# Kernel tuning notes

Measured on AMD Instinct MI355X. Metric: run time of the kernel, lower is better.

Reference implementation:

```python
import jax, jax.numpy as jnp
import numpy as np

IN_DIM = 128
OUT_DIM = 128
ATTN_DIM = 64
N_REL = 200
N_NODE = 50000
N_EDGE = 500000
N_QUERY = 64
COE_TIMEDIFF = 0.2  # computed in torch code but unused downstream


def setup_inputs() -> dict:
    key = jax.random.key(0)
    ks = jax.random.split(key, 24)
    # edges: [E,7] with columns (r_idx, _, rel, _, tau, sub, obj)
    r_idx = jax.random.randint(ks[0], (N_EDGE,), 0, N_QUERY)
    rel = jax.random.randint(ks[1], (N_EDGE,), 0, 2 * N_REL + 1)
    tau = jax.random.randint(ks[2], (N_EDGE,), -1, 366)  # -1 triggers the where() fallback
    sub = jax.random.randint(ks[3], (N_EDGE,), 0, N_NODE)
    obj = jax.random.randint(ks[4], (N_EDGE,), 0, N_NODE)
    fill = jnp.zeros((N_EDGE,), jnp.int64 if jax.config.jax_enable_x64 else jnp.int32)
    edges = jnp.stack([r_idx, fill, rel, fill, tau, sub, obj], axis=1)
    s = 1.0 / np.sqrt(IN_DIM)
    sa = 1.0 / np.sqrt(ATTN_DIM)
    return {
        "q_sub": jax.random.randint(ks[5], (N_QUERY,), 0, N_NODE),
        "q_rel": jax.random.randint(ks[6], (N_QUERY,), 0, 2 * N_REL + 1),
        "q_tau": jax.random.randint(ks[7], (N_QUERY,), 0, 366),
        "hidden": jax.random.normal(ks[8], (N_NODE, IN_DIM), jnp.float32),
        "edges": edges,
        "n_node": N_NODE,
        "old_nodes_new_idx": jax.random.randint(ks[9], (10000,), 0, N_NODE),
        "rela_embed": jax.random.normal(ks[10], (2 * N_REL + 1, IN_DIM), jnp.float32),
        "Ws": jax.random.normal(ks[11], (IN_DIM, ATTN_DIM), jnp.float32) * s,
        "Wr": jax.random.normal(ks[12], (IN_DIM, ATTN_DIM), jnp.float32) * s,
        "Wqr_W": jax.random.normal(ks[13], (IN_DIM, ATTN_DIM), jnp.float32) * s,
        "Wqr_b": jax.random.normal(ks[14], (ATTN_DIM,), jnp.float32) * s,
        "Wtau": jax.random.normal(ks[15], (IN_DIM, ATTN_DIM), jnp.float32) * s,
        "w_alpha_W": jax.random.normal(ks[16], (ATTN_DIM, 1), jnp.float32) * sa,
        "w_alpha_b": jax.random.normal(ks[17], (1,), jnp.float32) * sa,
        "Wh": jax.random.normal(ks[18], (IN_DIM, OUT_DIM), jnp.float32) * s,
        "wt1": jax.random.normal(ks[19], (1, IN_DIM), jnp.float32),
        "bt1": jax.random.normal(ks[20], (1, IN_DIM), jnp.float32),
        "wt2": jax.random.normal(ks[21], (1, IN_DIM), jnp.float32),
        "bt2": jax.random.normal(ks[22], (1, IN_DIM), jnp.float32),
    }


def reference(q_sub, q_rel, q_tau, hidden, edges, n_node, old_nodes_new_idx,
              rela_embed, Ws, Wr, Wqr_W, Wqr_b, Wtau, w_alpha_W, w_alpha_b,
              Wh, wt1, bt1, wt2, bt2):
    r_idx = edges[:, 0]
    rel = edges[:, 2]
    tau = edges[:, 4]
    sub = edges[:, 5]
    obj = edges[:, 6]
    hs = hidden[sub]                      # [E, in_dim] gather
    hr = rela_embed[rel]                  # [E, in_dim]
    h_qr = rela_embed[q_rel][r_idx]       # [E, in_dim]
    taus_q = q_tau[r_idx]
    tau = jnp.where(tau >= 0, tau, taus_q)
    delta_tau = (tau - taus_q).astype(hidden.dtype)[:, None]  # [E,1]
    h_tau = wt1 * delta_tau + bt1 + jnp.sin(wt2 * delta_tau + bt2)  # [E, in_dim]
    message = hs + hr + h_tau
    pre = jax.nn.relu(hs @ Ws + hr @ Wr + (h_qr @ Wqr_W + Wqr_b) + h_tau @ Wtau)
    alpha = jax.nn.sigmoid(pre @ w_alpha_W + w_alpha_b)  # [E,1]
    msg_agg = jax.ops.segment_sum(alpha * message, obj, num_segments=n_node)
    return msg_agg @ Wh  # act is identity by default
```

## Files before the change

### kernel.cpp

```cpp
#include <hip/hip_runtime.h>
#include <hip/hip_fp16.h>

#define IN_DIM   128
#define OUT_DIM  128
#define ATTN_DIM 64
#define N_RELV   401
#define N_NODE   50000
#define N_EDGE   500000
#define N_QUERY  64
#define N_DT     731
#define CAP      40

#define NB_NODE  782
#define NB_RELDT 566
#define NB_QR    32
#define NB_TOT   (NB_NODE + NB_RELDT + NB_QR + 1)

typedef unsigned short ushort_t;
typedef unsigned int   uint_t;
typedef __attribute__((ext_vector_type(8))) short v8s;
typedef __attribute__((ext_vector_type(4))) float v4f;

__device__ __forceinline__ int clampi(int v, int lo, int hi) {
    return v < lo ? lo : (v > hi ? hi : v);
}
__device__ __forceinline__ float bu2f(ushort_t u) {
    union { uint_t i; float f; } v; v.i = ((uint_t)u) << 16; return v.f;
}
__device__ __forceinline__ float blo(uint_t u) { return bu2f((ushort_t)(u & 0xffff)); }
__device__ __forceinline__ float bhi(uint_t u) { return bu2f((ushort_t)(u >> 16)); }
__device__ __forceinline__ ushort_t f2bu(float f) {
    union { float f; uint_t i; } v; v.f = f;
    const uint_t x = v.i;
    return (ushort_t)((x + 0x7fffu + ((x >> 16) & 1u)) >> 16);
}
__device__ __forceinline__ uint_t cvtpk(float a, float b) {
    uint_t r;
    asm("v_cvt_pk_bf16_f32 %0, %1, %2" : "=v"(r) : "v"(a), "v"(b));
    return r;
}

__device__ __forceinline__ void parse_edge(const int* __restrict__ edges, int e,
                                           int i64, int& r, int& rel, int& tau,
                                           int& sub, int& obj) {
    if (i64) {
        const int* E = edges + (size_t)e * 14;
        r = E[0]; rel = E[4]; tau = E[8]; sub = E[10]; obj = E[12];
    } else {
        const int* E = edges + (size_t)e * 7;
        r = E[0]; rel = E[2]; tau = E[4]; sub = E[5]; obj = E[6];
    }
    r   = clampi(r,   0, N_QUERY - 1);
    rel = clampi(rel, 0, N_RELV - 1);
    sub = clampi(sub, 0, N_NODE - 1);
    obj = clampi(obj, 0, N_NODE - 1);
}

__device__ __forceinline__ int swz_byte(int row, int byte_in_row) {
    return (row * 256 + byte_in_row) ^ ((row & 7) << 4);
}

__global__ __launch_bounds__(256) void fused_pre(
    const float* __restrict__ hidden, const float* __restrict__ Ws,
    const float* __restrict__ Wh,   const float* __restrict__ rela,
    const float* __restrict__ Wr,   const float* __restrict__ Wtau,
    const float* __restrict__ wt1,  const float* __restrict__ bt1,
    const float* __restrict__ wt2,  const float* __restrict__ bt2,
    const int* __restrict__ q_rel,  const float* __restrict__ WqrW,
    const float* __restrict__ Wqrb, const int* __restrict__ edges,
    ushort_t* __restrict__ node_attn, ushort_t* __restrict__ node_msg,
    ushort_t* __restrict__ rel_attn,  ushort_t* __restrict__ rel_msg,
    ushort_t* __restrict__ dt_attn,   ushort_t* __restrict__ dt_msg,
    ushort_t* __restrict__ Xqr,
    int* __restrict__ flag, int* __restrict__ cnt, int* __restrict__ ovfn)
{
    __shared__ ushort_t shw[192 * 128];
    const int bid = blockIdx.x, tid = threadIdx.x;

    if (bid < NB_NODE) {
        #pragma unroll
        for (int i = 0; i < 4; ++i) {
            const int pi = tid + 256 * i;
            const int kp = pi >> 4;
            const int n4 = (pi & 15) * 4;
            const float4 A = *(const float4*)(Ws + (size_t)(2 * kp) * 64 + n4);
            const float4 B = *(const float4*)(Ws + (size_t)(2 * kp + 1) * 64 + n4);
            const float Aa[4] = {A.x, A.y, A.z, A.w};
            const float Bа[4] = {B.x, B.y, B.z, B.w};
            #pragma unroll
            for (int j = 0; j < 4; ++j) {
                const int row = n4 + j;
                const uint_t u = (uint_t)f2bu(Aa[j]) | ((uint_t)f2bu(Bа[j]) << 16);
                *(uint_t*)((char*)shw + swz_byte(row, kp * 4)) = u;
            }
        }
        #pragma unroll
        for (int i = 0; i < 8; ++i) {
            const int pi = tid + 256 * i;
            const int kp = pi >> 5;
            const int n4 = (pi & 31) * 4;
            const float4 A = *(const float4*)(Wh + (size_t)(2 * kp) * 128 + n4);
            const float4 B = *(const float4*)(Wh + (size_t)(2 * kp + 1) * 128 + n4);
            const float Aa[4] = {A.x, A.y, A.z, A.w};
            const float Bа[4] = {B.x, B.y, B.z, B.w};
            #pragma unroll
            for (int j = 0; j < 4; ++j) {
                const int row = 64 + n4 + j;
                const uint_t u = (uint_t)f2bu(Aa[j]) | ((uint_t)f2bu(Bа[j]) << 16);
                *(uint_t*)((char*)shw + swz_byte(row, kp * 4)) = u;
            }
        }
        __syncthreads();

        const int wid  = tid >> 6;
        const int lane = tid & 63;
        const int m16  = lane & 15;
        const int q    = lane >> 4;
        const int nb   = bid * 64;
        const int row  = nb + wid * 16 + m16;
        const int rowc = row < N_NODE ? row : N_NODE - 1;

        v8s hfr[4];
        #pragma unroll
        for (int c = 0; c < 4; ++c) {
            const float4 f0 = *(const float4*)(hidden + (size_t)rowc * 128 + 32 * c + 8 * q);
            const float4 f1 = *(const float4*)(hidden + (size_t)rowc * 128 + 32 * c + 8 * q + 4);
            union { v8s s; uint4 u; } uu;
            uu.u = make_uint4(cvtpk(f0.x, f0.y), cvtpk(f0.z, f0.w),
                              cvtpk(f1.x, f1.y), cvtpk(f1.z, f1.w));
            hfr[c] = uu.s;
        }

        #pragma unroll
        for (int t = 0; t < 12; ++t) {
            v4f acc = {0.f, 0.f, 0.f, 0.f};
            #pragma unroll
            for (int c = 0; c < 4; ++c) {
                const v8s wfr = *(const v8s*)((const char*)shw +
                                  swz_byte(16 * t + m16, (32 * c + 8 * q) * 2));
                acc = __builtin_amdgcn_mfma_f32_16x16x32_bf16(wfr, hfr[c], acc, 0, 0, 0);
            }
            if (row < N_NODE) {
                const uint_t u0 = cvtpk(acc[0], acc[1]);
                const uint_t u1 = cvtpk(acc[2], acc[3]);
                const int dim = 16 * t + 4 * q;
                if (dim < 64) {
                    *(uint2*)(node_attn + (size_t)row * 64 + dim) = make_uint2(u0, u1);
                } else {
                    *(uint2*)(node_msg + (size_t)row * 128 + (dim - 64)) = make_uint2(u0, u1);
                }
            }
        }
    } else if (bid < NB_NODE + NB_RELDT) {
        const int bid2   = bid - NB_NODE;
        const int half   = tid >> 7;
        const int t128   = tid & 127;
        const int rowid  = bid2 * 2 + half;
        float* h = (float*)shw + half * 128;

        if (rowid < N_RELV) {
            h[t128] = rela[(size_t)rowid * IN_DIM + t128];
        } else {
            const float dtv = (float)((rowid - N_RELV) - 365);
            h[t128] = wt1[t128] * dtv + bt1[t128] + sinf(wt2[t128] * dtv + bt2[t128]);
        }
        __syncthreads();

        if (rowid < N_RELV) {
            if (t128 < ATTN_DIM) {
                float a = 0.f;
                #pragma unroll 8
                for (int d = 0; d < IN_DIM; ++d) a += h[d] * Wr[d * ATTN_DIM + t128];
                rel_attn[(size_t)rowid * ATTN_DIM + t128] = f2bu(a);
            }
            float m = 0.f;
            #pragma unroll 8
            for (int d = 0; d < IN_DIM; ++d) m += h[d] * Wh[d * OUT_DIM + t128];
            rel_msg[(size_t)rowid * OUT_DIM + t128] = f2bu(m);
        } else {
            const int i = rowid - N_RELV;
            if (t128 < ATTN_DIM) {
                float a = 0.f;
                #pragma unroll 8
                for (int d = 0; d < IN_DIM; ++d) a += h[d] * Wtau[d * ATTN_DIM + t128];
                dt_attn[(size_t)i * ATTN_DIM + t128] = f2bu(a);
            }
            float m = 0.f;
            #pragma unroll 8
            for (int d = 0; d < IN_DIM; ++d) m += h[d] * Wh[d * OUT_DIM + t128];
            dt_msg[(size_t)i * OUT_DIM + t128] = f2bu(m);
        }
        const int z = bid2 * 89 + tid;
        if (tid < 89 && z < N_NODE) cnt[z] = 0;
    } else if (bid < NB_NODE + NB_RELDT + NB_QR) {
        const int bid3 = bid - NB_NODE - NB_RELDT;
        const int half = tid >> 7;
        const int t128 = tid & 127;
        float* h  = (float*)shw + half * 128;
        int*   ok = (int*)((float*)shw + 512);

        if (tid == 0) *ok = 1;
        __syncthreads();
        const int w = edges[2 * tid + 1];
        if (w != 0 && w != -1) *ok = 0;
        __syncthreads();
        const int i64 = *ok;

        const int qn  = bid3 * 2 + half;
        const int rel = clampi(q_rel[i64 ? 2 * qn : qn], 0, N_RELV - 1);
        h[t128] = rela[(size_t)rel * IN_DIM + t128];
        __syncthreads();
        if (t128 < ATTN_DIM) {
            float acc = Wqrb[t128];
            #pragma unroll 8
            for (int d = 0; d < IN_DIM; ++d) acc += h[d] * WqrW[d * ATTN_DIM + t128];
            Xqr[(size_t)qn * ATTN_DIM + t128] = f2bu(acc);
        }
    } else {
        int* ok = (int*)shw;
        if (tid == 0) *ok = 0;
        __syncthreads();
        int badv = 0;
        for (int t = tid; t < 1000; t += 256) {
            const int w = edges[2 * t + 1];
            if (w != 0 && w != -1) badv = 1;
        }
        if (badv) *ok = 1;
        __syncthreads();
        if (tid == 0) { flag[0] = (*ok == 0) ? 1 : 0; ovfn[0] = 0; }
    }
}

__device__ __forceinline__ float dot8(uint4 xs, uint4 xr, uint4 xt, uint4 xq,
                                      float4 wA, float4 wB)
{
    float s0, s1, v;
    s0 = blo(xs.x) + blo(xr.x) + blo(xt.x) + blo(xq.x);
    s1 = bhi(xs.x) + bhi(xr.x) + bhi(xt.x) + bhi(xq.x);
    v  = fmaxf(s0, 0.f) * wA.x + fmaxf(s1, 0.f) * wA.y;
    s0 = blo(xs.y) + blo(xr.y) + blo(xt.y) + blo(xq.y);
    s1 = bhi(xs.y) + bhi(xr.y) + bhi(xt.y) + bhi(xq.y);
    v += fmaxf(s0, 0.f) * wA.z + fmaxf(s1, 0.f) * wA.w;
    s0 = blo(xs.z) + blo(xr.z) + blo(xt.z) + blo(xq.z);
    s1 = bhi(xs.z) + bhi(xr.z) + bhi(xt.z) + bhi(xq.z);
    v += fmaxf(s0, 0.f) * wB.x + fmaxf(s1, 0.f) * wB.y;
    s0 = blo(xs.w) + blo(xr.w) + blo(xt.w) + blo(xq.w);
    s1 = bhi(xs.w) + bhi(xr.w) + bhi(xt.w) + bhi(xq.w);
    v += fmaxf(s0, 0.f) * wB.z + fmaxf(s1, 0.f) * wB.w;
    return v;
}

__global__ __launch_bounds__(256) void alpha_scatter(
    const int* __restrict__ edges, const int* __restrict__ q_tau,
    const ushort_t* __restrict__ node_attn, const ushort_t* __restrict__ rel_attn,
    const ushort_t* __restrict__ dt_attn,  const ushort_t* __restrict__ Xqr,
    const float* __restrict__ w_alpha_W, const float* __restrict__ w_alpha_b,
    const int* __restrict__ flag, int* __restrict__ cnt,
    int2* __restrict__ meta, int* __restrict__ ovfn, int4* __restrict__ ovfl)
{
    const int g   = threadIdx.x & 7;
    const int grp = threadIdx.x >> 3;
    const int e0  = blockIdx.x * 128 + grp * 4;
    const int i64 = flag[0];

    const float4 wA = *(const float4*)(w_alpha_W + 8 * g);
    const float4 wB = *(const float4*)(w_alpha_W + 8 * g + 4);

    const int ec0 = e0     < N_EDGE ? e0     : N_EDGE - 1;
    const int ec1 = e0 + 1 < N_EDGE ? e0 + 1 : N_EDGE - 1;
    const int ec2 = e0 + 2 < N_EDGE ? e0 + 2 : N_EDGE - 1;
    const int ec3 = e0 + 3 < N_EDGE ? e0 + 3 : N_EDGE - 1;

    int r0, rel0, tau0, sub0, obj0; parse_edge(edges, ec0, i64, r0, rel0, tau0, sub0, obj0);
    int r1, rel1, tau1, sub1, obj1; parse_edge(edges, ec1, i64, r1, rel1, tau1, sub1, obj1);
    int r2, rel2, tau2, sub2, obj2; parse_edge(edges, ec2, i64, r2, rel2, tau2, sub2, obj2);
    int r3, rel3, tau3, sub3, obj3; parse_edge(edges, ec3, i64, r3, rel3, tau3, sub3, obj3);
    const int tq0 = q_tau[i64 ? 2 * r0 : r0];
    const int tq1 = q_tau[i64 ? 2 * r1 : r1];
    const int tq2 = q_tau[i64 ? 2 * r2 : r2];
    const int tq3 = q_tau[i64 ? 2 * r3 : r3];
    if (tau0 < 0) tau0 = tq0;
    if (tau1 < 0) tau1 = tq1;
    if (tau2 < 0) tau2 = tq2;
    if (tau3 < 0) tau3 = tq3;
    const int di0 = clampi(tau0 - tq0 + 365, 0, N_DT - 1);
    const int di1 = clampi(tau1 - tq1 + 365, 0, N_DT - 1);
    const int di2 = clampi(tau2 - tq2 + 365, 0, N_DT - 1);
    const int di3 = clampi(tau3 - tq3 + 365, 0, N_DT - 1);

    const uint4 xs0 = *(const uint4*)(node_attn + (size_t)sub0 * ATTN_DIM + 8 * g);
    const uint4 xr0 = *(const uint4*)(rel_attn + (size_t)rel0 * ATTN_DIM + 8 * g);
    const uint4 xt0 = *(const uint4*)(dt_attn  + (size_t)di0  * ATTN_DIM + 8 * g);
    const uint4 xq0 = *(const uint4*)(Xqr      + (size_t)r0   * ATTN_DIM + 8 * g);
    const uint4 xs1 = *(const uint4*)(node_attn + (size_t)sub1 * ATTN_DIM + 8 * g);
    const uint4 xr1 = *(const uint4*)(rel_attn + (size_t)rel1 * ATTN_DIM + 8 * g);
    const uint4 xt1 = *(const uint4*)(dt_attn  + (size_t)di1  * ATTN_DIM + 8 * g);
    const uint4 xq1 = *(const uint4*)(Xqr      + (size_t)r1   * ATTN_DIM + 8 * g);
    const uint4 xs2 = *(const uint4*)(node_attn + (size_t)sub2 * ATTN_DIM + 8 * g);
    const uint4 xr2 = *(const uint4*)(rel_attn + (size_t)rel2 * ATTN_DIM + 8 * g);
    const uint4 xt2 = *(const uint4*)(dt_attn  + (size_t)di2  * ATTN_DIM + 8 * g);
    const uint4 xq2 = *(const uint4*)(Xqr      + (size_t)r2   * ATTN_DIM + 8 * g);
    const uint4 xs3 = *(const uint4*)(node_attn + (size_t)sub3 * ATTN_DIM + 8 * g);
    const uint4 xr3 = *(const uint4*)(rel_attn + (size_t)rel3 * ATTN_DIM + 8 * g);
    const uint4 xt3 = *(const uint4*)(dt_attn  + (size_t)di3  * ATTN_DIM + 8 * g);
    const uint4 xq3 = *(const uint4*)(Xqr      + (size_t)r3   * ATTN_DIM + 8 * g);

    float v0 = dot8(xs0, xr0, xt0, xq0, wA, wB);
    float v1 = dot8(xs1, xr1, xt1, xq1, wA, wB);
    float v2 = dot8(xs2, xr2, xt2, xq2, wA, wB);
    float v3 = dot8(xs3, xr3, xt3, xq3, wA, wB);

    #pragma unroll
    for (int off = 4; off > 0; off >>= 1) {
        v0 += __shfl_xor(v0, off, 8);
        v1 += __shfl_xor(v1, off, 8);
        v2 += __shfl_xor(v2, off, 8);
        v3 += __shfl_xor(v3, off, 8);
    }

    if (g < 4 && e0 + g < N_EDGE) {
        const float vg  = g == 0 ? v0 : (g == 1 ? v1 : (g == 2 ? v2 : v3));
        const int objg  = g == 0 ? obj0 : (g == 1 ? obj1 : (g == 2 ? obj2 : obj3));
        const int subg  = g == 0 ? sub0 : (g == 1 ? sub1 : (g == 2 ? sub2 : sub3));
        const int dig   = g == 0 ? di0  : (g == 1 ? di1  : (g == 2 ? di2  : di3));
        const int relg  = g == 0 ? rel0 : (g == 1 ? rel1 : (g == 2 ? rel2 : rel3));
        const float alpha = 1.f / (1.f + __expf(-(vg + w_alpha_b[0])));
        const int pos = atomicAdd(&cnt[objg], 1);
        if (pos < CAP) {
            const uint_t px = (uint_t)subg | ((uint_t)dig << 17) | ((uint_t)(relg & 31) << 27);
            const uint_t py = (uint_t)(relg >> 5) |
                              ((uint_t)__half_as_ushort(__float2half_rn(alpha)) << 16);
            meta[(size_t)pos * N_NODE + objg] = make_int2((int)px, (int)py);
        } else {
            const int ov = atomicAdd(ovfn, 1);
            if (ov < N_EDGE)
                ovfl[ov] = make_int4(subg | (dig << 17), relg | (objg << 9),
                                     __float_as_int(alpha), 0);
        }
    }
}

__device__ __forceinline__ void agg_edge(
    int2 m, int l32,
    const ushort_t* __restrict__ node_msg, const ushort_t* __restrict__ rel_msg,
    const ushort_t* __restrict__ dt_msg,
    float& a0, float& a1, float& a2, float& a3)
{
    const int sub = m.x & 0x1FFFF;
    const int di  = ((uint_t)m.x >> 17) & 0x3FF;
    const int rel = (((uint_t)m.x >> 27) & 31) | (((uint_t)m.y & 0xF) << 5);
    const float al = __half2float(__ushort_as_half((ushort_t)((uint_t)m.y >> 16)));
    const uint2 am = *(const uint2*)(node_msg + (size_t)sub * 128 + 4 * l32);
    const uint2 bm = *(const uint2*)(rel_msg  + (size_t)rel * 128 + 4 * l32);
    const uint2 tm = *(const uint2*)(dt_msg   + (size_t)di  * 128 + 4 * l32);
    a0 += al * (blo(am.x) + blo(bm.x) + blo(tm.x));
    a1 += al * (bhi(am.x) + bhi(bm.x) + bhi(tm.x));
    a2 += al * (blo(am.y) + blo(bm.y) + blo(tm.y));
    a3 += al * (bhi(am.y) + bhi(bm.y) + bhi(tm.y));
}

__global__ __launch_bounds__(256) void agg_kernel(
    const int* __restrict__ cnt, const int2* __restrict__ meta,
    const int* __restrict__ ovfn, const int4* __restrict__ ovfl,
    const ushort_t* __restrict__ node_msg, const ushort_t* __restrict__ rel_msg,
    const ushort_t* __restrict__ dt_msg, float* __restrict__ out)
{
    const int lane = threadIdx.x & 63;
    const int half = lane >> 5;
    const int l32  = lane & 31;
    const int n    = blockIdx.x * 4 + (threadIdx.x >> 6);

    int m = cnt[n]; if (m > CAP) m = CAP;
    float a0 = 0.f, a1 = 0.f, a2 = 0.f, a3 = 0.f;

    int j = 0;
    for (; j + 3 < m; j += 4) {
        const int2 ma = meta[(size_t)(j + half) * N_NODE + n];
        const int2 mb = meta[(size_t)(j + 2 + half) * N_NODE + n];
        agg_edge(ma, l32, node_msg, rel_msg, dt_msg, a0, a1, a2, a3);
        agg_edge(mb, l32, node_msg, rel_msg, dt_msg, a0, a1, a2, a3);
    }
    for (; j + 1 < m; j += 2) {
        const int2 ma = meta[(size_t)(j + half) * N_NODE + n];
        agg_edge(ma, l32, node_msg, rel_msg, dt_msg, a0, a1, a2, a3);
    }
    if (j < m && half == 0) {
        const int2 ma = meta[(size_t)j * N_NODE + n];
        agg_edge(ma, l32, node_msg, rel_msg, dt_msg, a0, a1, a2, a3);
    }

    int nov = ovfn[0]; if (nov > N_EDGE) nov = N_EDGE;
    for (int i = 0; i < nov; ++i) {
        const int4 mo = ovfl[i];
        const int objo = (int)((uint_t)mo.y >> 9);
        if (objo != n || half != 0) continue;
        const int subo = mo.x & 0x1FFFF;
        const int dio  = (int)((uint_t)mo.x >> 17);
        const int relo = mo.y & 0x1FF;
        const float alo = __int_as_float(mo.z);
        const uint2 am = *(const uint2*)(node_msg + (size_t)subo * 128 + 4 * l32);
        const uint2 bm = *(const uint2*)(rel_msg  + (size_t)relo * 128 + 4 * l32);
        const uint2 tm = *(const uint2*)(dt_msg   + (size_t)dio  * 128 + 4 * l32);
        a0 += alo * (blo(am.x) + blo(bm.x) + blo(tm.x));
        a1 += alo * (bhi(am.x) + bhi(bm.x) + bhi(tm.x));
        a2 += alo * (blo(am.y) + blo(bm.y) + blo(tm.y));
        a3 += alo * (bhi(am.y) + bhi(bm.y) + bhi(tm.y));
    }

    a0 += __shfl_xor(a0, 32, 64);
    a1 += __shfl_xor(a1, 32, 64);
    a2 += __shfl_xor(a2, 32, 64);
    a3 += __shfl_xor(a3, 32, 64);

    if (half == 0) {
        float4 o; o.x = a0; o.y = a1; o.z = a2; o.w = a3;
        *(float4*)(out + (size_t)n * OUT_DIM + 4 * l32) = o;
    }
}

__global__ __launch_bounds__(256) void edge_atomic_kernel(
    const int* __restrict__ edges, const int* __restrict__ q_tau,
    const ushort_t* __restrict__ node_attn, const ushort_t* __restrict__ node_msg,
    const ushort_t* __restrict__ rel_attn,  const ushort_t* __restrict__ rel_msg,
    const ushort_t* __restrict__ dt_attn,   const ushort_t* __restrict__ dt_msg,
    const ushort_t* __restrict__ Xqr,
    const float* __restrict__ w_alpha_W, const float* __restrict__ w_alpha_b,
    const int* __restrict__ flag, float* __restrict__ out)
{
    const int lane = threadIdx.x & 63;
    const int e    = blockIdx.x * 4 + (threadIdx.x >> 6);
    const int i64  = flag[0];

    int r, rel, tau, sub, obj;
    parse_edge(edges, e, i64, r, rel, tau, sub, obj);
    const int tq = q_tau[i64 ? 2 * r : r];
    if (tau < 0) tau = tq;
    const int di = clampi(tau - tq + 365, 0, N_DT - 1);

    const float xs = bu2f(node_attn[(size_t)sub * ATTN_DIM + lane]);
    const float xr = bu2f(rel_attn[(size_t)rel * ATTN_DIM + lane]);
    const float xt = bu2f(dt_attn[(size_t)di  * ATTN_DIM + lane]);
    const float xq = bu2f(Xqr[(size_t)r * ATTN_DIM + lane]);

    float v = fmaxf(xs + xr + xq + xt, 0.f) * w_alpha_W[lane];
    #pragma unroll
    for (int off = 32; off > 0; off >>= 1)
        v += __shfl_down(v, off, 64);
    v = __shfl(v, 0, 64);
    const float alpha = 1.f / (1.f + __expf(-(v + w_alpha_b[0])));

    const uint_t am = *(const uint_t*)(node_msg + (size_t)sub * 128 + 2 * lane);
    const uint_t bm = *(const uint_t*)(rel_msg  + (size_t)rel * 128 + 2 * lane);
    const uint_t tm = *(const uint_t*)(dt_msg   + (size_t)di  * 128 + 2 * lane);
    const float mx = blo(am) + blo(bm) + blo(tm);
    const float my = bhi(am) + bhi(bm) + bhi(tm);

    float* dst = out + (size_t)obj * OUT_DIM;
    atomicAdd(dst + 2 * lane,     alpha * mx);
    atomicAdd(dst + 2 * lane + 1, alpha * my);
}

extern "C" void kernel_launch(void* const* d_in, const int* in_sizes, int n_in,
                              void* d_out, int out_size, void* d_ws, size_t ws_size,
                              hipStream_t stream)
{
    const int*   q_rel  = (const int*)d_in[1];
    const int*   q_tau  = (const int*)d_in[2];
    const float* hidden = (const float*)d_in[3];
    const int*   edges  = (const int*)d_in[4];
    const float* rela   = (const float*)d_in[7];
    const float* Ws     = (const float*)d_in[8];
    const float* Wr     = (const float*)d_in[9];
    const float* WqrW   = (const float*)d_in[10];
    const float* Wqrb   = (const float*)d_in[11];
    const float* Wtau   = (const float*)d_in[12];
    const float* waW    = (const float*)d_in[13];
    const float* wab    = (const float*)d_in[14];
    const float* Wh     = (const float*)d_in[15];
    const float* wt1    = (const float*)d_in[16];
    const float* bt1    = (const float*)d_in[17];
    const float* wt2    = (const float*)d_in[18];
    const float* bt2    = (const float*)d_in[19];
    float* out = (float*)d_out;

    char* p = (char*)d_ws;
    size_t off = 0;
    auto carve = [&](size_t bytes) {
        char* q = p + off;
        off = (off + bytes + 255) & ~(size_t)255;
        return q;
    };
    int*      flag      = (int*)     carve(64);
    int*      cnt       = (int*)     carve((size_t)N_NODE * 4);
    int*      ovfn      = (int*)     carve(64);
    ushort_t* XqrB      = (ushort_t*)carve((size_t)N_QUERY * ATTN_DIM * 2);
    ushort_t* rel_attn  = (ushort_t*)carve((size_t)N_RELV * ATTN_DIM * 2);
    ushort_t* rel_msg   = (ushort_t*)carve((size_t)N_RELV * OUT_DIM * 2);
    ushort_t* dt_attn   = (ushort_t*)carve((size_t)N_DT * ATTN_DIM * 2);
    ushort_t* dt_msg    = (ushort_t*)carve((size_t)N_DT * OUT_DIM * 2);
    ushort_t* node_attn = (ushort_t*)carve((size_t)N_NODE * ATTN_DIM * 2);
    ushort_t* node_msg  = (ushort_t*)carve((size_t)N_NODE * OUT_DIM * 2);
    int2*     meta      = (int2*)    carve((size_t)N_NODE * CAP * 8);
    int4*     ovfl      = (int4*)    carve((size_t)N_EDGE * 16);
    const size_t need_full = off;

    fused_pre<<<NB_TOT, 256, 0, stream>>>(
        hidden, Ws, Wh, rela, Wr, Wtau, wt1, bt1, wt2, bt2,
        q_rel, WqrW, Wqrb, edges,
        node_attn, node_msg, rel_attn, rel_msg, dt_attn, dt_msg, XqrB,
        flag, cnt, ovfn);

    if (ws_size >= need_full) {
        alpha_scatter<<<(N_EDGE + 127) / 128, 256, 0, stream>>>(
            edges, q_tau, node_attn, rel_attn, dt_attn, XqrB,
            waW, wab, flag, cnt, meta, ovfn, ovfl);
        agg_kernel<<<N_NODE / 4, 256, 0, stream>>>(cnt, meta, ovfn, ovfl,
                                                   node_msg, rel_msg, dt_msg, out);
    } else {
        (void)hipMemsetAsync(out, 0, (size_t)out_size * sizeof(float), stream);
        edge_atomic_kernel<<<N_EDGE / 4, 256, 0, stream>>>(edges, q_tau,
                                                           node_attn, node_msg,
                                                           rel_attn, rel_msg,
                                                           dt_attn, dt_msg, XqrB,
                                                           waW, wab, flag, out);
    }
}
```

Measured before the change: 200.2 us.

## Move relation, time-delta and query projections onto MFMA and vectorize edge loads

The scalar per-row dot-product blocks for relation, time-delta and query projections are replaced with MFMA bf16 tiles that reuse the node-projection path. Fewer blocks handle these tables and the count buffer is zeroed with int4 stores. The edge kernel reads each group's 4 edges with one int4 load per lane plus shuffles instead of scalar strided loads. The aggregation loop is unrolled to 8 edges. Projections of the small tables now run in bf16 rather than fp32, which slightly changes precision, and the i64 format check now samples more edges.

```diff
diff --git a/kernel.cpp b/kernel.cpp
--- a/kernel.cpp
+++ b/kernel.cpp
@@ -11,10 +11,17 @@
 #define N_DT     731
 #define CAP      40
 
-#define NB_NODE  782
-#define NB_RELDT 566
-#define NB_QR    32
-#define NB_TOT   (NB_NODE + NB_RELDT + NB_QR + 1)
+#define NBW_NODE 782
+#define NBW_REL  7
+#define NBW_DT   12
+#define NBW_QR   1
+#define NBW_ZERO 13
+#define RB0      NBW_NODE
+#define DB0      (NBW_NODE + NBW_REL)
+#define QB0      (DB0 + NBW_DT)
+#define ZB0      (QB0 + NBW_QR)
+#define FB0      (ZB0 + NBW_ZERO)
+#define NB_TOT   (FB0 + 1)
 
 typedef unsigned short ushort_t;
 typedef unsigned int   uint_t;
@@ -40,24 +47,78 @@
     return r;
 }
 
-__device__ __forceinline__ void parse_edge(const int* __restrict__ edges, int e,
-                                           int i64, int& r, int& rel, int& tau,
-                                           int& sub, int& obj) {
-    if (i64) {
-        const int* E = edges + (size_t)e * 14;
-        r = E[0]; rel = E[4]; tau = E[8]; sub = E[10]; obj = E[12];
-    } else {
-        const int* E = edges + (size_t)e * 7;
-        r = E[0]; rel = E[2]; tau = E[4]; sub = E[5]; obj = E[6];
-    }
-    r   = clampi(r,   0, N_QUERY - 1);
-    rel = clampi(rel, 0, N_RELV - 1);
-    sub = clampi(sub, 0, N_NODE - 1);
-    obj = clampi(obj, 0, N_NODE - 1);
-}
-
 __device__ __forceinline__ int swz_byte(int row, int byte_in_row) {
     return (row * 256 + byte_in_row) ^ ((row & 7) << 4);
+}
+
+__device__ __forceinline__ void stage_w64(ushort_t* shw, const float* __restrict__ W,
+                                          int tid) {
+    #pragma unroll
+    for (int i = 0; i < 4; ++i) {
+        const int pi = tid + 256 * i;
+        const int kp = pi >> 4;
+        const int n4 = (pi & 15) * 4;
+        const float4 A = *(const float4*)(W + (size_t)(2 * kp) * 64 + n4);
+        const float4 B = *(const float4*)(W + (size_t)(2 * kp + 1) * 64 + n4);
+        const float Aa[4] = {A.x, A.y, A.z, A.w};
+        const float Ba[4] = {B.x, B.y, B.z, B.w};
+        #pragma unroll
+        for (int j = 0; j < 4; ++j)
+            *(uint_t*)((char*)shw + swz_byte(n4 + j, kp * 4)) = cvtpk(Aa[j], Ba[j]);
+    }
+}
+__device__ __forceinline__ void stage_w128(ushort_t* shw, const float* __restrict__ W,
+                                           int tid) {
+    #pragma unroll
+    for (int i = 0; i < 8; ++i) {
+        const int pi = tid + 256 * i;
+        const int kp = pi >> 5;
+        const int n4 = (pi & 31) * 4;
+        const float4 A = *(const float4*)(W + (size_t)(2 * kp) * 128 + n4);
+        const float4 B = *(const float4*)(W + (size_t)(2 * kp + 1) * 128 + n4);
+        const float Aa[4] = {A.x, A.y, A.z, A.w};
+        const float Ba[4] = {B.x, B.y, B.z, B.w};
+        #pragma unroll
+        for (int j = 0; j < 4; ++j)
+            *(uint_t*)((char*)shw + swz_byte(64 + n4 + j, kp * 4)) = cvtpk(Aa[j], Ba[j]);
+    }
+}
+__device__ __forceinline__ void load_x_rows(const float* __restrict__ X, int rowc,
+                                            int q, v8s hfr[4]) {
+    #pragma unroll
+    for (int c = 0; c < 4; ++c) {
+        const float4 f0 = *(const float4*)(X + (size_t)rowc * 128 + 32 * c + 8 * q);
+        const float4 f1 = *(const float4*)(X + (size_t)rowc * 128 + 32 * c + 8 * q + 4);
+        union { v8s s; uint4 u; } uu;
+        uu.u = make_uint4(cvtpk(f0.x, f0.y), cvtpk(f0.z, f0.w),
+                          cvtpk(f1.x, f1.y), cvtpk(f1.z, f1.w));
+        hfr[c] = uu.s;
+    }
+}
+__device__ __forceinline__ void mfma_store(const ushort_t* shw, const v8s hfr[4],
+                                           int row, int Nlim,
+                                           ushort_t* __restrict__ attn_out,
+                                           ushort_t* __restrict__ msg_out,
+                                           int m16, int q) {
+    #pragma unroll
+    for (int t = 0; t < 12; ++t) {
+        v4f acc = {0.f, 0.f, 0.f, 0.f};
+        #pragma unroll
+        for (int c = 0; c < 4; ++c) {
+            const v8s wfr = *(const v8s*)((const char*)shw +
+                              swz_byte(16 * t + m16, (32 * c + 8 * q) * 2));
+            acc = __builtin_amdgcn_mfma_f32_16x16x32_bf16(wfr, hfr[c], acc, 0, 0, 0);
+        }
+        if (row < Nlim) {
+            const uint_t u0 = cvtpk(acc[0], acc[1]);
+            const uint_t u1 = cvtpk(acc[2], acc[3]);
+            const int dim = 16 * t + 4 * q;
+            if (dim < 64)
+                *(uint2*)(attn_out + (size_t)row * 64 + dim) = make_uint2(u0, u1);
+            else
+                *(uint2*)(msg_out + (size_t)row * 128 + (dim - 64)) = make_uint2(u0, u1);
+        }
+    }
 }
 
 __global__ __launch_bounds__(256) void fused_pre(
@@ -76,63 +137,77 @@
 {
     __shared__ ushort_t shw[192 * 128];
     const int bid = blockIdx.x, tid = threadIdx.x;
-
-    if (bid < NB_NODE) {
-        #pragma unroll
-        for (int i = 0; i < 4; ++i) {
-            const int pi = tid + 256 * i;
-            const int kp = pi >> 4;
-            const int n4 = (pi & 15) * 4;
-            const float4 A = *(const float4*)(Ws + (size_t)(2 * kp) * 64 + n4);
-            const float4 B = *(const float4*)(Ws + (size_t)(2 * kp + 1) * 64 + n4);
-            const float Aa[4] = {A.x, A.y, A.z, A.w};
-            const float Bа[4] = {B.x, B.y, B.z, B.w};
-            #pragma unroll
-            for (int j = 0; j < 4; ++j) {
-                const int row = n4 + j;
-                const uint_t u = (uint_t)f2bu(Aa[j]) | ((uint_t)f2bu(Bа[j]) << 16);
-                *(uint_t*)((char*)shw + swz_byte(row, kp * 4)) = u;
-            }
-        }
-        #pragma unroll
-        for (int i = 0; i < 8; ++i) {
-            const int pi = tid + 256 * i;
-            const int kp = pi >> 5;
-            const int n4 = (pi & 31) * 4;
-            const float4 A = *(const float4*)(Wh + (size_t)(2 * kp) * 128 + n4);
-            const float4 B = *(const float4*)(Wh + (size_t)(2 * kp + 1) * 128 + n4);
-            const float Aa[4] = {A.x, A.y, A.z, A.w};
-            const float Bа[4] = {B.x, B.y, B.z, B.w};
-            #pragma unroll
-            for (int j = 0; j < 4; ++j) {
-                const int row = 64 + n4 + j;
-                const uint_t u = (uint_t)f2bu(Aa[j]) | ((uint_t)f2bu(Bа[j]) << 16);
-                *(uint_t*)((char*)shw + swz_byte(row, kp * 4)) = u;
-            }
-        }
-        __syncthreads();
-
-        const int wid  = tid >> 6;
-        const int lane = tid & 63;
-        const int m16  = lane & 15;
-        const int q    = lane >> 4;
-        const int nb   = bid * 64;
-        const int row  = nb + wid * 16 + m16;
+    const int wid = tid >> 6, lane = tid & 63;
+    const int m16 = lane & 15, q = lane >> 4;
+
+    if (bid < NBW_NODE) {
+        stage_w64 (shw, Ws, tid);
+        stage_w128(shw, Wh, tid);
+        __syncthreads();
+        const int row  = bid * 64 + wid * 16 + m16;
         const int rowc = row < N_NODE ? row : N_NODE - 1;
-
+        v8s hfr[4];
+        load_x_rows(hidden, rowc, q, hfr);
+        mfma_store(shw, hfr, row, N_NODE, node_attn, node_msg, m16, q);
+    } else if (bid < DB0) {
+        stage_w64 (shw, Wr, tid);
+        stage_w128(shw, Wh, tid);
+        __syncthreads();
+        const int row  = (bid - RB0) * 64 + wid * 16 + m16;
+        const int rowc = row < N_RELV ? row : N_RELV - 1;
+        v8s hfr[4];
+        load_x_rows(rela, rowc, q, hfr);
+        mfma_store(shw, hfr, row, N_RELV, rel_attn, rel_msg, m16, q);
+    } else if (bid < QB0) {
+        stage_w64 (shw, Wtau, tid);
+        stage_w128(shw, Wh, tid);
+        __syncthreads();
+        const int row  = (bid - DB0) * 64 + wid * 16 + m16;
+        const int rowc = row < N_DT ? row : N_DT - 1;
+        const float dtv = (float)(rowc - 365);
         v8s hfr[4];
         #pragma unroll
         for (int c = 0; c < 4; ++c) {
-            const float4 f0 = *(const float4*)(hidden + (size_t)rowc * 128 + 32 * c + 8 * q);
-            const float4 f1 = *(const float4*)(hidden + (size_t)rowc * 128 + 32 * c + 8 * q + 4);
+            const int o = 32 * c + 8 * q;
+            const float4 w1a = *(const float4*)(wt1 + o), w1b = *(const float4*)(wt1 + o + 4);
+            const float4 b1a = *(const float4*)(bt1 + o), b1b = *(const float4*)(bt1 + o + 4);
+            const float4 w2a = *(const float4*)(wt2 + o), w2b = *(const float4*)(wt2 + o + 4);
+            const float4 b2a = *(const float4*)(bt2 + o), b2b = *(const float4*)(bt2 + o + 4);
+            const float h0 = w1a.x * dtv + b1a.x + sinf(w2a.x * dtv + b2a.x);
+            const float h1 = w1a.y * dtv + b1a.y + sinf(w2a.y * dtv + b2a.y);
+            const float h2 = w1a.z * dtv + b1a.z + sinf(w2a.z * dtv + b2a.z);
+            const float h3 = w1a.w * dtv + b1a.w + sinf(w2a.w * dtv + b2a.w);
+            const float h4 = w1b.x * dtv + b1b.x + sinf(w2b.x * dtv + b2b.x);
+            const float h5 = w1b.y * dtv + b1b.y + sinf(w2b.y * dtv + b2b.y);
+            const float h6 = w1b.z * dtv + b1b.z + sinf(w2b.z * dtv + b2b.z);
+            const float h7 = w1b.w * dtv + b1b.w + sinf(w2b.w * dtv + b2b.w);
             union { v8s s; uint4 u; } uu;
-            uu.u = make_uint4(cvtpk(f0.x, f0.y), cvtpk(f0.z, f0.w),
-                              cvtpk(f1.x, f1.y), cvtpk(f1.z, f1.w));
+            uu.u = make_uint4(cvtpk(h0, h1), cvtpk(h2, h3), cvtpk(h4, h5), cvtpk(h6, h7));
             hfr[c] = uu.s;
         }
-
+        mfma_store(shw, hfr, row, N_DT, dt_attn, dt_msg, m16, q);
+    } else if (bid < ZB0) {
+        int* ok = (int*)shw;
+        if (tid == 0) *ok = 1;
+        __syncthreads();
+        int badv = 0;
+        for (int t = tid; t < 1000; t += 256) {
+            const int w = edges[2 * t + 1];
+            if (w != 0 && w != -1) badv = 1;
+        }
+        if (badv) *ok = 0;
+        __syncthreads();
+        const int i64 = *ok;
+        __syncthreads();
+
+        stage_w64(shw, WqrW, tid);
+        __syncthreads();
+        const int qrow = wid * 16 + m16;
+        const int relq = clampi(q_rel[i64 ? 2 * qrow : qrow], 0, N_RELV - 1);
+        v8s hfr[4];
+        load_x_rows(rela, relq, q, hfr);
         #pragma unroll
-        for (int t = 0; t < 12; ++t) {
+        for (int t = 0; t < 4; ++t) {
             v4f acc = {0.f, 0.f, 0.f, 0.f};
             #pragma unroll
             for (int c = 0; c < 4; ++c) {
@@ -140,81 +215,19 @@
                                   swz_byte(16 * t + m16, (32 * c + 8 * q) * 2));
                 acc = __builtin_amdgcn_mfma_f32_16x16x32_bf16(wfr, hfr[c], acc, 0, 0, 0);
             }
-            if (row < N_NODE) {
-                const uint_t u0 = cvtpk(acc[0], acc[1]);
-                const uint_t u1 = cvtpk(acc[2], acc[3]);
-                const int dim = 16 * t + 4 * q;
-                if (dim < 64) {
-                    *(uint2*)(node_attn + (size_t)row * 64 + dim) = make_uint2(u0, u1);
-                } else {
-                    *(uint2*)(node_msg + (size_t)row * 128 + (dim - 64)) = make_uint2(u0, u1);
-                }
-            }
-        }
-    } else if (bid < NB_NODE + NB_RELDT) {
-        const int bid2   = bid - NB_NODE;
-        const int half   = tid >> 7;
-        const int t128   = tid & 127;
-        const int rowid  = bid2 * 2 + half;
-        float* h = (float*)shw + half * 128;
-
-        if (rowid < N_RELV) {
-            h[t128] = rela[(size_t)rowid * IN_DIM + t128];
-        } else {
-            const float dtv = (float)((rowid - N_RELV) - 365);
-            h[t128] = wt1[t128] * dtv + bt1[t128] + sinf(wt2[t128] * dtv + bt2[t128]);
-        }
-        __syncthreads();
-
-        if (rowid < N_RELV) {
-            if (t128 < ATTN_DIM) {
-                float a = 0.f;
-                #pragma unroll 8
-                for (int d = 0; d < IN_DIM; ++d) a += h[d] * Wr[d * ATTN_DIM + t128];
-                rel_attn[(size_t)rowid * ATTN_DIM + t128] = f2bu(a);
-            }
-            float m = 0.f;
-            #pragma unroll 8
-            for (int d = 0; d < IN_DIM; ++d) m += h[d] * Wh[d * OUT_DIM + t128];
-            rel_msg[(size_t)rowid * OUT_DIM + t128] = f2bu(m);
-        } else {
-            const int i = rowid - N_RELV;
-            if (t128 < ATTN_DIM) {
-                float a = 0.f;
-                #pragma unroll 8
-                for (int d = 0; d < IN_DIM; ++d) a += h[d] * Wtau[d * ATTN_DIM + t128];
-                dt_attn[(size_t)i * ATTN_DIM + t128] = f2bu(a);
-            }
-            float m = 0.f;
-            #pragma unroll 8
-            for (int d = 0; d < IN_DIM; ++d) m += h[d] * Wh[d * OUT_DIM + t128];
-            dt_msg[(size_t)i * OUT_DIM + t128] = f2bu(m);
-        }
-        const int z = bid2 * 89 + tid;
-        if (tid < 89 && z < N_NODE) cnt[z] = 0;
-    } else if (bid < NB_NODE + NB_RELDT + NB_QR) {
-        const int bid3 = bid - NB_NODE - NB_RELDT;
-        const int half = tid >> 7;
-        const int t128 = tid & 127;
-        float* h  = (float*)shw + half * 128;
-        int*   ok = (int*)((float*)shw + 512);
-
-        if (tid == 0) *ok = 1;
-        __syncthreads();
-        const int w = edges[2 * tid + 1];
-        if (w != 0 && w != -1) *ok = 0;
-        __syncthreads();
-        const int i64 = *ok;
-
-        const int qn  = bid3 * 2 + half;
-        const int rel = clampi(q_rel[i64 ? 2 * qn : qn], 0, N_RELV - 1);
-        h[t128] = rela[(size_t)rel * IN_DIM + t128];
-        __syncthreads();
-        if (t128 < ATTN_DIM) {
-            float acc = Wqrb[t128];
-            #pragma unroll 8
-            for (int d = 0; d < IN_DIM; ++d) acc += h[d] * WqrW[d * ATTN_DIM + t128];
-            Xqr[(size_t)qn * ATTN_DIM + t128] = f2bu(acc);
+            const int dim = 16 * t + 4 * q;
+            const float4 bi = *(const float4*)(Wqrb + dim);
+            const uint_t u0 = cvtpk(acc[0] + bi.x, acc[1] + bi.y);
+            const uint_t u1 = cvtpk(acc[2] + bi.z, acc[3] + bi.w);
+            *(uint2*)(Xqr + (size_t)qrow * 64 + dim) = make_uint2(u0, u1);
+        }
+    } else if (bid < FB0) {
+        int4* c4 = (int4*)cnt;
+        const int b = (bid - ZB0) * 256 + tid;
+        #pragma unroll
+        for (int k = 0; k < 4; ++k) {
+            const int i4 = b * 4 + k;
+            if (i4 < N_NODE / 4) c4[i4] = make_int4(0, 0, 0, 0);
         }
     } else {
         int* ok = (int*)shw;
@@ -260,21 +273,43 @@
 {
     const int g   = threadIdx.x & 7;
     const int grp = threadIdx.x >> 3;
-    const int e0  = blockIdx.x * 128 + grp * 4;
+    const int e0r = blockIdx.x * 128 + grp * 4;
+    const int e0  = e0r <= N_EDGE - 4 ? e0r : N_EDGE - 4;
     const int i64 = flag[0];
 
     const float4 wA = *(const float4*)(w_alpha_W + 8 * g);
     const float4 wB = *(const float4*)(w_alpha_W + 8 * g + 4);
 
-    const int ec0 = e0     < N_EDGE ? e0     : N_EDGE - 1;
-    const int ec1 = e0 + 1 < N_EDGE ? e0 + 1 : N_EDGE - 1;
-    const int ec2 = e0 + 2 < N_EDGE ? e0 + 2 : N_EDGE - 1;
-    const int ec3 = e0 + 3 < N_EDGE ? e0 + 3 : N_EDGE - 1;
-
-    int r0, rel0, tau0, sub0, obj0; parse_edge(edges, ec0, i64, r0, rel0, tau0, sub0, obj0);
-    int r1, rel1, tau1, sub1, obj1; parse_edge(edges, ec1, i64, r1, rel1, tau1, sub1, obj1);
-    int r2, rel2, tau2, sub2, obj2; parse_edge(edges, ec2, i64, r2, rel2, tau2, sub2, obj2);
-    int r3, rel3, tau3, sub3, obj3; parse_edge(edges, ec3, i64, r3, rel3, tau3, sub3, obj3);
+    int r0, rel0, tau0, sub0, obj0, r1, rel1, tau1, sub1, obj1;
+    int r2, rel2, tau2, sub2, obj2, r3, rel3, tau3, sub3, obj3;
+    if (!i64) {
+        const int4 ev = *(const int4*)(edges + (size_t)e0 * 7 + 4 * (g < 6 ? g : 6));
+        #define GETF(j) __shfl(((j) & 3) == 0 ? ev.x : ((j) & 3) == 1 ? ev.y : \
+                               ((j) & 3) == 2 ? ev.z : ev.w, (j) >> 2, 8)
+        r0 = GETF(0);  rel0 = GETF(2);  tau0 = GETF(4);  sub0 = GETF(5);  obj0 = GETF(6);
+        r1 = GETF(7);  rel1 = GETF(9);  tau1 = GETF(11); sub1 = GETF(12); obj1 = GETF(13);
+        r2 = GETF(14); rel2 = GETF(16); tau2 = GETF(18); sub2 = GETF(19); obj2 = GETF(20);
+        r3 = GETF(21); rel3 = GETF(23); tau3 = GETF(25); sub3 = GETF(26); obj3 = GETF(27);
+        #undef GETF
+    } else {
+        const int* E0 = edges + (size_t)(e0    ) * 14;
+        const int* E1 = edges + (size_t)(e0 + 1) * 14;
+        const int* E2 = edges + (size_t)(e0 + 2) * 14;
+        const int* E3 = edges + (size_t)(e0 + 3) * 14;
+        r0 = E0[0]; rel0 = E0[4]; tau0 = E0[8]; sub0 = E0[10]; obj0 = E0[12];
+        r1 = E1[0]; rel1 = E1[4]; tau1 = E1[8]; sub1 = E1[10]; obj1 = E1[12];
+        r2 = E2[0]; rel2 = E2[4]; tau2 = E2[8]; sub2 = E2[10]; obj2 = E2[12];
+        r3 = E3[0]; rel3 = E3[4]; tau3 = E3[8]; sub3 = E3[10]; obj3 = E3[12];
+    }
+    r0 = clampi(r0, 0, N_QUERY - 1); rel0 = clampi(rel0, 0, N_RELV - 1);
+    sub0 = clampi(sub0, 0, N_NODE - 1); obj0 = clampi(obj0, 0, N_NODE - 1);
+    r1 = clampi(r1, 0, N_QUERY - 1); rel1 = clampi(rel1, 0, N_RELV - 1);
+    sub1 = clampi(sub1, 0, N_NODE - 1); obj1 = clampi(obj1, 0, N_NODE - 1);
+    r2 = clampi(r2, 0, N_QUERY - 1); rel2 = clampi(rel2, 0, N_RELV - 1);
+    sub2 = clampi(sub2, 0, N_NODE - 1); obj2 = clampi(obj2, 0, N_NODE - 1);
+    r3 = clampi(r3, 0, N_QUERY - 1); rel3 = clampi(rel3, 0, N_RELV - 1);
+    sub3 = clampi(sub3, 0, N_NODE - 1); obj3 = clampi(obj3, 0, N_NODE - 1);
+
     const int tq0 = q_tau[i64 ? 2 * r0 : r0];
     const int tq1 = q_tau[i64 ? 2 * r1 : r1];
     const int tq2 = q_tau[i64 ? 2 * r2 : r2];
@@ -318,7 +353,7 @@
         v3 += __shfl_xor(v3, off, 8);
     }
 
-    if (g < 4 && e0 + g < N_EDGE) {
+    if (g < 4 && e0r + g < N_EDGE) {
         const float vg  = g == 0 ? v0 : (g == 1 ? v1 : (g == 2 ? v2 : v3));
         const int objg  = g == 0 ? obj0 : (g == 1 ? obj1 : (g == 2 ? obj2 : obj3));
         const int subg  = g == 0 ? sub0 : (g == 1 ? sub1 : (g == 2 ? sub2 : sub3));
@@ -374,11 +409,15 @@
     float a0 = 0.f, a1 = 0.f, a2 = 0.f, a3 = 0.f;
 
     int j = 0;
-    for (; j + 3 < m; j += 4) {
-        const int2 ma = meta[(size_t)(j + half) * N_NODE + n];
+    for (; j + 7 < m; j += 8) {
+        const int2 ma = meta[(size_t)(j     + half) * N_NODE + n];
         const int2 mb = meta[(size_t)(j + 2 + half) * N_NODE + n];
+        const int2 mc = meta[(size_t)(j + 4 + half) * N_NODE + n];
+        const int2 md = meta[(size_t)(j + 6 + half) * N_NODE + n];
         agg_edge(ma, l32, node_msg, rel_msg, dt_msg, a0, a1, a2, a3);
         agg_edge(mb, l32, node_msg, rel_msg, dt_msg, a0, a1, a2, a3);
+        agg_edge(mc, l32, node_msg, rel_msg, dt_msg, a0, a1, a2, a3);
+        agg_edge(md, l32, node_msg, rel_msg, dt_msg, a0, a1, a2, a3);
     }
     for (; j + 1 < m; j += 2) {
         const int2 ma = meta[(size_t)(j + half) * N_NODE + n];
@@ -416,6 +455,22 @@
         float4 o; o.x = a0; o.y = a1; o.z = a2; o.w = a3;
         *(float4*)(out + (size_t)n * OUT_DIM + 4 * l32) = o;
     }
+}
+
+__device__ __forceinline__ void parse_edge(const int* __restrict__ edges, int e,
+                                           int i64, int& r, int& rel, int& tau,
+                                           int& sub, int& obj) {
+    if (i64) {
+        const int* E = edges + (size_t)e * 14;
+        r = E[0]; rel = E[4]; tau = E[8]; sub = E[10]; obj = E[12];
+    } else {
+        const int* E = edges + (size_t)e * 7;
+        r = E[0]; rel = E[2]; tau = E[4]; sub = E[5]; obj = E[6];
+    }
+    r   = clampi(r,   0, N_QUERY - 1);
+    rel = clampi(rel, 0, N_RELV - 1);
+    sub = clampi(sub, 0, N_NODE - 1);
+    obj = clampi(obj, 0, N_NODE - 1);
 }
 
 __global__ __launch_bounds__(256) void edge_atomic_kernel(
```

Result: no change. 197.8 us (-1.2%).
